# Kernel tuning notes

Measured on AMD Instinct MI355X. Metric: run time of the kernel, lower is better.

## Reference

```python
import jax, jax.numpy as jnp
import numpy as np

VOCAB, EMBED, MAXLEN, UNITS, F1, BATCH = 50000, 256, 512, 32, 16, 512

def setup_inputs() -> dict:
    key = jax.random.key(0)
    ks = jax.random.split(key, 9)
    tokens = jax.random.randint(ks[0], (BATCH, MAXLEN), 0, VOCAB, dtype=jnp.int32)
    emb_table = jax.random.normal(ks[1], (VOCAB, EMBED), dtype=jnp.float32) * 0.02
    # SimpleRNN params (Keras: kernel, recurrent_kernel, bias)
    Wx = jax.random.normal(ks[2], (EMBED, UNITS), dtype=jnp.float32) * (1.0 / np.sqrt(EMBED))
    Wh = jax.random.normal(ks[3], (UNITS, UNITS), dtype=jnp.float32) * (1.0 / np.sqrt(UNITS))
    b  = jnp.zeros((UNITS,), dtype=jnp.float32)
    W1 = jax.random.normal(ks[4], (UNITS, F1), dtype=jnp.float32) * (1.0 / np.sqrt(UNITS))
    b1 = jnp.zeros((F1,), dtype=jnp.float32)
    W2 = jax.random.normal(ks[5], (F1, 1), dtype=jnp.float32) * (1.0 / np.sqrt(F1))
    b2 = jnp.zeros((1,), dtype=jnp.float32)
    return {"tokens": tokens, "emb_table": emb_table, "Wx": Wx, "Wh": Wh, "b": b,
            "W1": W1, "b1": b1, "W2": W2, "b2": b2}

def reference(tokens, emb_table, Wx, Wh, b, W1, b1, W2, b2):
    # Embedding lookup: [B, T, E]
    x = emb_table[tokens]
    # SimpleRNN recurrence (tanh), return last hidden state. Dropout disabled (inference).
    xs = jnp.transpose(x, (1, 0, 2))  # time-major [T, B, E]
    h0 = jnp.zeros((tokens.shape[0], Wh.shape[0]), dtype=x.dtype)

    def step(h, x_t):
        h_new = jnp.tanh(x_t @ Wx + h @ Wh + b)
        return h_new, None

    h_last, _ = jax.lax.scan(step, h0, xs)
    # Flatten is a no-op on [B, 32]; Dense heads are linear (no activation), then sigmoid.
    z = (h_last @ W1 + b1) @ W2 + b2
    return jax.nn.sigmoid(z)  # [B, 1]
```

## Files before the change

### kernel.cpp

```cpp
#include <hip/hip_runtime.h>
#include <hip/hip_bf16.h>
#include <math.h>

#define TT 512
#define BB 512
#define EE 256
#define UU 32
#define FF1 16
#define NWAVE 2048

#define TWO_LOG2E 2.8853900817779268f

__device__ __forceinline__ float rdlane(float v, int lane) {
    return __int_as_float(__builtin_amdgcn_readlane(__float_as_int(v), lane));
}

#define DPP_ADD(v, ctrl)                                                    \
    (v) += __int_as_float(__builtin_amdgcn_update_dpp(                      \
        0, __float_as_int(v), (ctrl), 0xf, 0xf, true))

__global__ __launch_bounds__(64) void proj_dpp(
    const float* __restrict__ emb, const float* __restrict__ Wx,
    const float* __restrict__ bias, float* __restrict__ P, int nrows)
{
    const int L = threadIdx.x;
    const int g = L >> 4;
    const int c = L & 15;
    const int wv = blockIdx.x;

    float w[16][8];
    #pragma unroll
    for (int kk = 0; kk < 16; ++kk) {
        const float4* src = (const float4*)(Wx + (size_t)(kk * 16 + c) * UU + g * 8);
        float4 a = src[0], b = src[1];
        w[kk][0] = a.x; w[kk][1] = a.y; w[kk][2] = a.z; w[kk][3] = a.w;
        w[kk][4] = b.x; w[kk][5] = b.y; w[kk][6] = b.z; w[kk][7] = b.w;
    }
    float bs[8];
    #pragma unroll
    for (int uu = 0; uu < 8; ++uu) bs[uu] = bias[g * 8 + uu];

    auto rowptr = [&](int i) {
        int r = wv + NWAVE * i;
        if (r >= nrows) r = nrows - 1;
        return emb + (size_t)r * EE;
    };

    float xA[16], xB[16];
    {
        const float* rp = rowptr(0);
        #pragma unroll
        for (int kk = 0; kk < 16; ++kk) xA[kk] = rp[kk * 16 + c];
    }

    const int NI = (nrows - 1 - wv) / NWAVE + 1;

    for (int i = 0; i < NI; ++i) {
        {
            const float* rp = rowptr(i + 1 < NI ? i + 1 : i);
            #pragma unroll
            for (int kk = 0; kk < 16; ++kk) xB[kk] = rp[kk * 16 + c];
        }

        float p[8];
        #pragma unroll
        for (int uu = 0; uu < 8; ++uu) p[uu] = 0.f;
        #pragma unroll
        for (int kk = 0; kk < 16; ++kk) {
            const float xk = xA[kk];
            #pragma unroll
            for (int uu = 0; uu < 8; ++uu)
                p[uu] = fmaf(xk, w[kk][uu], p[uu]);
        }

        #pragma unroll
        for (int uu = 0; uu < 8; ++uu) {
            DPP_ADD(p[uu], 0x111);
            DPP_ADD(p[uu], 0x112);
            DPP_ADD(p[uu], 0x114);
            DPP_ADD(p[uu], 0x118);
        }

        if (c == 15) {
            const int r = wv + NWAVE * i;
            float4 o0, o1;
            o0.x = (p[0] + bs[0]) * TWO_LOG2E;
            o0.y = (p[1] + bs[1]) * TWO_LOG2E;
            o0.z = (p[2] + bs[2]) * TWO_LOG2E;
            o0.w = (p[3] + bs[3]) * TWO_LOG2E;
            o1.x = (p[4] + bs[4]) * TWO_LOG2E;
            o1.y = (p[5] + bs[5]) * TWO_LOG2E;
            o1.z = (p[6] + bs[6]) * TWO_LOG2E;
            o1.w = (p[7] + bs[7]) * TWO_LOG2E;
            float4* dst = (float4*)(P + (size_t)r * UU + g * 8);
            dst[0] = o0; dst[1] = o1;
        }

        #pragma unroll
        for (int kk = 0; kk < 16; ++kk) xA[kk] = xB[kk];
    }
}

__global__ __launch_bounds__(64) void scan_heads(
    const int* __restrict__ tokens, const float* __restrict__ P,
    const float* __restrict__ Wh,
    const float* __restrict__ W1, const float* __restrict__ b1,
    const float* __restrict__ W2, const float* __restrict__ b2,
    float* __restrict__ out)
{
    __shared__ float xs[TT * UU];

    const int L = threadIdx.x;
    const int u = L & 31;
    const int b = blockIdx.x;
    const int* trow = tokens + b * TT;

    float wh[UU];
    #pragma unroll
    for (int k = 0; k < UU; ++k) wh[k] = Wh[k * UU + u] * TWO_LOG2E;

    const int sub = L >> 3;
    const int q   = L & 7;
    for (int c = 0; c < 8; ++c) {
        int tk8[8];
        #pragma unroll
        for (int i = 0; i < 8; ++i)
            tk8[i] = trow[c * 64 + i * 8 + sub];
        #pragma unroll
        for (int i = 0; i < 8; ++i) {
            const float* src = P + (size_t)tk8[i] * UU + q * 4;
            float* dst = xs + (c * 64 + i * 8) * UU;
            __builtin_amdgcn_global_load_lds(
                (const __attribute__((address_space(1))) void*)src,
                (__attribute__((address_space(3))) void*)dst, 16, 0, 0);
        }
    }
    __syncthreads();

    float xr[8];
    #pragma unroll
    for (int j = 0; j < 8; ++j) xr[j] = xs[j * UU + u];

    float h = 0.f;

    for (int t = 0; t < TT; t += 8) {
        float xn[8];
        #pragma unroll
        for (int j = 0; j < 8; ++j)
            xn[j] = xs[((t + 8 + j) & (TT - 1)) * UU + u];

        #pragma unroll
        for (int j = 0; j < 8; ++j) {
            float hv[UU];
            #pragma unroll
            for (int k = 0; k < UU; ++k) hv[k] = rdlane(h, k);

            float a0 = fmaf(hv[0], wh[0], xr[j]);
            float a1 = hv[1] * wh[1];
            float a2 = hv[2] * wh[2];
            float a3 = hv[3] * wh[3];
            #pragma unroll
            for (int k = 4; k < UU; k += 4) {
                a0 = fmaf(hv[k],     wh[k],     a0);
                a1 = fmaf(hv[k + 1], wh[k + 1], a1);
                a2 = fmaf(hv[k + 2], wh[k + 2], a2);
                a3 = fmaf(hv[k + 3], wh[k + 3], a3);
            }
            float e = __builtin_amdgcn_exp2f((a0 + a1) + (a2 + a3));
            float r = __builtin_amdgcn_rcpf(e + 1.0f);
            h = fmaf(-2.0f, r, 1.0f);
            xr[j] = xn[j];
        }
    }

    const int j = threadIdx.x & 15;
    float s = b1[j];
    #pragma unroll
    for (int k = 0; k < UU; ++k) {
        float hk = rdlane(h, k);
        s = fmaf(hk, W1[k * FF1 + j], s);
    }
    float z = b2[0];
    #pragma unroll
    for (int jj = 0; jj < FF1; ++jj) {
        float yj = rdlane(s, jj);
        z = fmaf(yj, W2[jj], z);
    }
    if (threadIdx.x == 0) {
        float e = __builtin_amdgcn_exp2f(-z * 1.4426950408889634f);
        out[b] = __builtin_amdgcn_rcpf(1.0f + e);
    }
}

extern "C" void kernel_launch(void* const* d_in, const int* in_sizes, int n_in,
                              void* d_out, int out_size, void* d_ws, size_t ws_size,
                              hipStream_t stream) {
    const int*   tokens = (const int*)  d_in[0];
    const float* emb    = (const float*)d_in[1];
    const float* Wx     = (const float*)d_in[2];
    const float* Wh     = (const float*)d_in[3];
    const float* bias   = (const float*)d_in[4];
    const float* W1     = (const float*)d_in[5];
    const float* b1     = (const float*)d_in[6];
    const float* W2     = (const float*)d_in[7];
    const float* b2     = (const float*)d_in[8];
    float* out = (float*)d_out;

    const int vocab = in_sizes[1] / EE;
    float* P = (float*)d_ws;

    proj_dpp<<<dim3(NWAVE), dim3(64), 0, stream>>>(
        emb, Wx, bias, P, vocab);

    scan_heads<<<dim3(BB), dim3(64), 0, stream>>>(
        tokens, P, Wh, W1, b1, W2, b2, out);
}
```

Before: 183.3 us.

## Replace per-step readlane broadcasts with permlane32 swap and DPP row_ror FMAs

The recurrent matvec no longer broadcasts each of the 32 hidden values with v_readlane. Instead it remaps units so that each 16-lane row holds 16 units, swaps the two wave halves with v_permlane32_swap, and feeds the rotated h values straight into v_fmac through DPP row_ror modifiers. A runtime probe finds the rotation direction so the pre-rotated Wh registers line up with the right lanes. This targets the serial readlane latency on the critical path of every scan step, at the cost of hand-written inline asm with manual s_nop hazard padding.

```diff
diff --git a/kernel.cpp b/kernel.cpp
--- a/kernel.cpp
+++ b/kernel.cpp
@@ -111,25 +111,33 @@
     __shared__ float xs[TT * UU];
 
     const int L = threadIdx.x;
-    const int u = L & 31;
+    const int c = L & 15;
+    const int u = c + ((L >> 5) << 4);
     const int b = blockIdx.x;
     const int* trow = tokens + b * TT;
 
-    float wh[UU];
-    #pragma unroll
-    for (int k = 0; k < UU; ++k) wh[k] = Wh[k * UU + u] * TWO_LOG2E;
+    int probe = __builtin_amdgcn_update_dpp(0, c, 0x121, 0xf, 0xf, true);
+    const int kstep = (__builtin_amdgcn_readfirstlane(probe) == 15) ? -1 : 1;
+
+    float wA[16], wB[16];
+    #pragma unroll
+    for (int jj = 0; jj < 16; ++jj) {
+        const int kj = (c + kstep * jj) & 15;
+        wA[jj] = TWO_LOG2E * Wh[kj * UU + u];
+        wB[jj] = TWO_LOG2E * Wh[(16 + kj) * UU + u];
+    }
 
     const int sub = L >> 3;
     const int q   = L & 7;
-    for (int c = 0; c < 8; ++c) {
+    for (int cc = 0; cc < 8; ++cc) {
         int tk8[8];
         #pragma unroll
         for (int i = 0; i < 8; ++i)
-            tk8[i] = trow[c * 64 + i * 8 + sub];
+            tk8[i] = trow[cc * 64 + i * 8 + sub];
         #pragma unroll
         for (int i = 0; i < 8; ++i) {
             const float* src = P + (size_t)tk8[i] * UU + q * 4;
-            float* dst = xs + (c * 64 + i * 8) * UU;
+            float* dst = xs + (cc * 64 + i * 8) * UU;
             __builtin_amdgcn_global_load_lds(
                 (const __attribute__((address_space(1))) void*)src,
                 (__attribute__((address_space(3))) void*)dst, 16, 0, 0);
@@ -151,21 +159,60 @@
 
         #pragma unroll
         for (int j = 0; j < 8; ++j) {
-            float hv[UU];
-            #pragma unroll
-            for (int k = 0; k < UU; ++k) hv[k] = rdlane(h, k);
-
-            float a0 = fmaf(hv[0], wh[0], xr[j]);
-            float a1 = hv[1] * wh[1];
-            float a2 = hv[2] * wh[2];
-            float a3 = hv[3] * wh[3];
-            #pragma unroll
-            for (int k = 4; k < UU; k += 4) {
-                a0 = fmaf(hv[k],     wh[k],     a0);
-                a1 = fmaf(hv[k + 1], wh[k + 1], a1);
-                a2 = fmaf(hv[k + 2], wh[k + 2], a2);
-                a3 = fmaf(hv[k + 3], wh[k + 3], a3);
-            }
+            float A  = h;
+            float Bv = h;
+            asm("s_nop 1\n\t"
+                "v_permlane32_swap_b32 %0, %1\n\t"
+                "s_nop 1"
+                : "+v"(A), "+v"(Bv));
+
+            float a0, a1, a2, a3;
+            asm("v_fma_f32  %0, %4, %6, %5\n\t"
+                "v_mul_f32  %1, %4, %7  row_ror:1\n\t"
+                "v_mul_f32  %2, %4, %8  row_ror:2\n\t"
+                "v_mul_f32  %3, %4, %9  row_ror:3\n\t"
+                "v_fmac_f32 %0, %4, %10 row_ror:4\n\t"
+                "v_fmac_f32 %1, %4, %11 row_ror:5\n\t"
+                "v_fmac_f32 %2, %4, %12 row_ror:6\n\t"
+                "v_fmac_f32 %3, %4, %13 row_ror:7\n\t"
+                "v_fmac_f32 %0, %4, %14 row_ror:8\n\t"
+                "v_fmac_f32 %1, %4, %15 row_ror:9\n\t"
+                "v_fmac_f32 %2, %4, %16 row_ror:10\n\t"
+                "v_fmac_f32 %3, %4, %17 row_ror:11\n\t"
+                "v_fmac_f32 %0, %4, %18 row_ror:12\n\t"
+                "v_fmac_f32 %1, %4, %19 row_ror:13\n\t"
+                "v_fmac_f32 %2, %4, %20 row_ror:14\n\t"
+                "v_fmac_f32 %3, %4, %21 row_ror:15"
+                : "=&v"(a0), "=&v"(a1), "=&v"(a2), "=&v"(a3)
+                : "v"(A), "v"(xr[j]),
+                  "v"(wA[0]),  "v"(wA[1]),  "v"(wA[2]),  "v"(wA[3]),
+                  "v"(wA[4]),  "v"(wA[5]),  "v"(wA[6]),  "v"(wA[7]),
+                  "v"(wA[8]),  "v"(wA[9]),  "v"(wA[10]), "v"(wA[11]),
+                  "v"(wA[12]), "v"(wA[13]), "v"(wA[14]), "v"(wA[15]));
+
+            asm("v_fmac_f32 %0, %4, %5\n\t"
+                "v_fmac_f32 %1, %4, %6  row_ror:1\n\t"
+                "v_fmac_f32 %2, %4, %7  row_ror:2\n\t"
+                "v_fmac_f32 %3, %4, %8  row_ror:3\n\t"
+                "v_fmac_f32 %0, %4, %9  row_ror:4\n\t"
+                "v_fmac_f32 %1, %4, %10 row_ror:5\n\t"
+                "v_fmac_f32 %2, %4, %11 row_ror:6\n\t"
+                "v_fmac_f32 %3, %4, %12 row_ror:7\n\t"
+                "v_fmac_f32 %0, %4, %13 row_ror:8\n\t"
+                "v_fmac_f32 %1, %4, %14 row_ror:9\n\t"
+                "v_fmac_f32 %2, %4, %15 row_ror:10\n\t"
+                "v_fmac_f32 %3, %4, %16 row_ror:11\n\t"
+                "v_fmac_f32 %0, %4, %17 row_ror:12\n\t"
+                "v_fmac_f32 %1, %4, %18 row_ror:13\n\t"
+                "v_fmac_f32 %2, %4, %19 row_ror:14\n\t"
+                "v_fmac_f32 %3, %4, %20 row_ror:15"
+                : "+v"(a0), "+v"(a1), "+v"(a2), "+v"(a3)
+                : "v"(Bv),
+                  "v"(wB[0]),  "v"(wB[1]),  "v"(wB[2]),  "v"(wB[3]),
+                  "v"(wB[4]),  "v"(wB[5]),  "v"(wB[6]),  "v"(wB[7]),
+                  "v"(wB[8]),  "v"(wB[9]),  "v"(wB[10]), "v"(wB[11]),
+                  "v"(wB[12]), "v"(wB[13]), "v"(wB[14]), "v"(wB[15]));
+
             float e = __builtin_amdgcn_exp2f((a0 + a1) + (a2 + a3));
             float r = __builtin_amdgcn_rcpf(e + 1.0f);
             h = fmaf(-2.0f, r, 1.0f);
@@ -173,12 +220,12 @@
         }
     }
 
-    const int j = threadIdx.x & 15;
-    float s = b1[j];
+    const int jh = L & 15;
+    float s = b1[jh];
     #pragma unroll
     for (int k = 0; k < UU; ++k) {
-        float hk = rdlane(h, k);
-        s = fmaf(hk, W1[k * FF1 + j], s);
+        float hk = rdlane(h, (k & 15) + ((k >> 4) << 5));
+        s = fmaf(hk, W1[k * FF1 + jh], s);
     }
     float z = b2[0];
     #pragma unroll
@@ -186,7 +233,7 @@
         float yj = rdlane(s, jj);
         z = fmaf(yj, W2[jj], z);
     }
-    if (threadIdx.x == 0) {
+    if (L == 0) {
         float e = __builtin_amdgcn_exp2f(-z * 1.4426950408889634f);
         out[b] = __builtin_amdgcn_rcpf(1.0f + e);
     }
```

Result: faster. 175.2 us (-4.4%).
